# Performance work log

Measured on AMD Instinct MI355X. Metric: run time of the kernel, lower is better.

## Reference

```python
import jax, jax.numpy as jnp
import numpy as np

# dims matching init_kwargs / input_specs
B, C, H = 8, 256, 48          # input (B, C, H, H)
GRID = 3                       # sqrt(num_memory)
NUM_MEM = GRID * GRID          # 9
WS = H // GRID                 # window_size = 16
S = 128                        # num_slots
D = WS * WS * C                # slot_dim = 65536
K = 5                          # gumbel top-k threshold (shrink_thres, int)
EPS = 1e-12


def setup_inputs() -> dict:
    key = jax.random.key(0)
    k1, k2, k3 = jax.random.split(key, 3)
    stdv = 1.0 / np.sqrt(D)
    x = jax.random.normal(k1, (B, C, H, H), dtype=jnp.float32)
    mem1 = jax.random.uniform(k2, (NUM_MEM, S, D), jnp.float32, -stdv, stdv)
    mem2 = jax.random.uniform(k3, (NUM_MEM, S, D), jnp.float32, -stdv, stdv)
    return {"x": x, "mem1": mem1, "mem2": mem2}


def _window_partition(x):
    # (B, C, H, W) -> (B, NUM_MEM, WS*WS*C); per-window layout is (ws, ws, C) row-major,
    # matching torch unfold -> view(B,C,ws^2,L) -> permute(0,3,2,1).
    b = x.shape[0]
    x = jnp.transpose(x, (0, 2, 3, 1))                        # (B, H, W, C)
    x = x.reshape(b, GRID, WS, GRID, WS, C)
    x = jnp.transpose(x, (0, 1, 3, 2, 4, 5))                  # (B, gh, gw, ws, ws, C)
    return x.reshape(b, NUM_MEM, WS * WS * C)


def _window_reverse(w):
    # (B, NUM_MEM, WS*WS*C) -> (B, C, H, W); exact inverse of _window_partition.
    b = w.shape[0]
    w = w.reshape(b, GRID, GRID, WS, WS, C)
    w = jnp.transpose(w, (0, 1, 3, 2, 4, 5)).reshape(b, H, H, C)
    return jnp.transpose(w, (0, 3, 1, 2))


def _hard_shrink_relu(y, lambd):
    d = y - lambd
    return jax.nn.relu(d) * y / (jnp.abs(d) + EPS)


def _memory_read(q, mem):
    # q: (B, M, D) window queries; mem: (M, S, D) per-window memory matrices.
    att = jnp.einsum('bmd,msd->bms', q, mem)                  # (B, M, S)
    y = jax.nn.softmax(att, axis=-1)
    k = min(S - 1, K)
    thres = jax.lax.top_k(y, k)[0][..., -1:]                  # kth largest per row
    y_hard = _hard_shrink_relu(y, thres)
    y_hard = y_hard / jnp.maximum(jnp.sum(jnp.abs(y_hard), axis=-1, keepdims=True), EPS)
    y_hard = jax.lax.stop_gradient(y_hard - y) + y            # straight-through
    return jnp.einsum('bms,msd->bmd', y_hard, mem)            # (B, M, D)


def reference(x, mem1, mem2):
    # CRU modeled as identity split: x1 = x2 = x (CRU source not provided).
    q = _window_partition(x)                                  # (B, 9, D)
    out1 = _window_reverse(_memory_read(q, mem1))
    out2 = _window_reverse(_memory_read(q, mem2))
    return out1 + out2                                        # eval mode: no bernoulli mask
```

## Files before the change

kernel.cpp:

```cpp
#include <hip/hip_runtime.h>
#include <hip/hip_bf16.h>
#include <cstdint>

#define Bn 8
#define Cn 256
#define Hn 48
#define NUM_MEM 9
#define WSZ 16
#define Sn 128
#define Dn 65536
#define KTOP 5
#define NDC 128

__global__ __launch_bounds__(256) void k_x2q(const float* __restrict__ x,
                                             float* __restrict__ q) {
    const int h = blockIdx.x;
    const int b = blockIdx.y;
    const int gh = h >> 4, i = h & 15;
    __shared__ float tile[Cn * Hn];
    const float* xp = x + (size_t)b * Cn * Hn * Hn + (size_t)h * Hn;
    for (int o = threadIdx.x; o < Cn * Hn; o += blockDim.x) {
        int c = o / Hn, w = o - c * Hn;
        tile[o] = xp[(size_t)c * Hn * Hn + w];
    }
    __syncthreads();
    for (int gw = 0; gw < 3; ++gw) {
        float* qp = q + (size_t)(b * NUM_MEM + gh * 3 + gw) * Dn + i * (WSZ * Cn);
        for (int l = threadIdx.x; l < WSZ * Cn; l += blockDim.x) {
            int j = l >> 8, c = l & 255;
            qp[l] = tile[c * Hn + gw * WSZ + j];
        }
    }
}

__global__ __launch_bounds__(256) void k_att4(const float* __restrict__ q,
                                              const float* __restrict__ mem1,
                                              const float* __restrict__ mem2,
                                              float* __restrict__ ap) {
    const int dc = blockIdx.x;
    const int mw = blockIdx.y;
    const int sg = blockIdx.z;
    const int e  = sg >> 3;
    const int lane = threadIdx.x & 63, wave = threadIdx.x >> 6;
    const int s0 = (sg & 7) * 16 + wave * 4;

    const float4* mem4 = (const float4*)(e ? mem2 : mem1);
    const float4* q4   = (const float4*)q;
    const int off = dc * 128 + lane;

    float4 M[4][2];
#pragma unroll
    for (int r = 0; r < 4; ++r) {
        const float4* mp = mem4 + (size_t)(mw * Sn + s0 + r) * (Dn / 4) + off;
        M[r][0] = mp[0];
        M[r][1] = mp[64];
    }

    float a[32];
#pragma unroll
    for (int i = 0; i < 32; ++i) a[i] = 0.f;

#pragma unroll
    for (int half = 0; half < 2; ++half) {
        float4 Q[4][2];
#pragma unroll
        for (int b = 0; b < 4; ++b) {
            const float4* qp = q4 + (size_t)((half * 4 + b) * NUM_MEM + mw) * (Dn / 4) + off;
            Q[b][0] = qp[0];
            Q[b][1] = qp[64];
        }
#pragma unroll
        for (int r = 0; r < 4; ++r)
#pragma unroll
            for (int b = 0; b < 4; ++b) {
                const int bi = half * 4 + b;
                a[r * 8 + bi] += M[r][0].x * Q[b][0].x + M[r][0].y * Q[b][0].y
                               + M[r][0].z * Q[b][0].z + M[r][0].w * Q[b][0].w
                               + M[r][1].x * Q[b][1].x + M[r][1].y * Q[b][1].y
                               + M[r][1].z * Q[b][1].z + M[r][1].w * Q[b][1].w;
            }
    }

#pragma unroll
    for (int k = 0; k < 5; ++k) {
        const int mk = 1 << k;
        const bool up = (lane & mk) != 0;
#pragma unroll
        for (int j = 0; j < (32 >> (k + 1)); ++j) {
            float lo = a[2 * j], hi = a[2 * j + 1];
            float mine = up ? hi : lo;
            float oth  = __shfl_xor(up ? lo : hi, mk, 64);
            a[j] = mine + oth;
        }
    }
    float rsum = a[0] + __shfl_xor(a[0], 32, 64);
    if (lane < 32) {
        const int b = lane & 7, r = (lane >> 3) & 3;
        ap[((size_t)dc * 144 + (size_t)(e * 8 + b) * 9 + mw) * Sn + (s0 + r)] = rsum;
    }
}

__global__ __launch_bounds__(128) void k_smax(const float* __restrict__ ap,
                                              float* __restrict__ w) {
    const int row = blockIdx.x;
    const int t = threadIdx.x;
    __shared__ float sf[Sn];
    __shared__ unsigned long long sk[Sn];

    float v = 0.f;
#pragma unroll 8
    for (int nd = 0; nd < NDC; ++nd)
        v += ap[((size_t)nd * 144 + row) * Sn + t];

    sf[t] = v; __syncthreads();
    for (int s = 64; s > 0; s >>= 1) { if (t < s) sf[t] = fmaxf(sf[t], sf[t + s]); __syncthreads(); }
    float mx = sf[0]; __syncthreads();

    float e = expf(v - mx);
    sf[t] = e; __syncthreads();
    for (int s = 64; s > 0; s >>= 1) { if (t < s) sf[t] += sf[t + s]; __syncthreads(); }
    float sum = sf[0]; __syncthreads();
    float y = e / sum;

    bool alive = true;
    float thres = 0.f;
    unsigned int ybits = __float_as_uint(y);
    for (int it = 0; it < KTOP; ++it) {
        sk[t] = alive ? ((((unsigned long long)ybits) << 32) | (unsigned)t) : 0ull;
        __syncthreads();
        for (int s = 64; s > 0; s >>= 1) {
            if (t < s) { if (sk[t + s] > sk[t]) sk[t] = sk[t + s]; }
            __syncthreads();
        }
        unsigned long long kmax = sk[0];
        __syncthreads();
        if ((unsigned)(kmax & 0xffffffffull) == (unsigned)t) alive = false;
        thres = __uint_as_float((unsigned)(kmax >> 32));
    }

    float d   = y - thres;
    float num = fmaxf(d, 0.f) * y;
    float yh  = num / (fabsf(d) + 1e-12f);

    sf[t] = yh; __syncthreads();
    for (int s = 64; s > 0; s >>= 1) { if (t < s) sf[t] += sf[t + s]; __syncthreads(); }
    float l1 = sf[0];
    w[(size_t)row * Sn + t] = yh / fmaxf(l1, 1e-12f);
}

__global__ __launch_bounds__(256) void k_acc(const float* __restrict__ w,
                                             const float* __restrict__ mem1,
                                             const float* __restrict__ mem2,
                                             float* __restrict__ acc) {
    const int chunk = blockIdx.x;
    const int m     = blockIdx.y;
    const int b     = blockIdx.z;
    __shared__ int   nz[2];
    __shared__ int   idx[2][16];
    __shared__ float wv[2][16];
    if (threadIdx.x < 2) nz[threadIdx.x] = 0;
    __syncthreads();
    {
        int eidx = threadIdx.x >> 7;
        int s    = threadIdx.x & 127;
        float ww = w[((size_t)(eidx * Bn + b) * NUM_MEM + m) * Sn + s];
        if (ww != 0.f) {
            int p = atomicAdd(&nz[eidx], 1);
            if (p < 16) { idx[eidx][p] = s; wv[eidx][p] = ww; }
        }
    }
    __syncthreads();
    const int n1 = nz[0], n2 = nz[1];
    const size_t mbase = (size_t)m * Sn * Dn;
    const int dbase = chunk * 4096;
    for (int l = threadIdx.x * 4; l < 4096; l += 1024) {
        int d = dbase + l;
        float4 a = {0.f, 0.f, 0.f, 0.f};
        for (int j = 0; j < n1; ++j) {
            const float4 r = *(const float4*)(mem1 + mbase + (size_t)idx[0][j] * Dn + d);
            float ww = wv[0][j];
            a.x += ww * r.x; a.y += ww * r.y; a.z += ww * r.z; a.w += ww * r.w;
        }
        for (int j = 0; j < n2; ++j) {
            const float4 r = *(const float4*)(mem2 + mbase + (size_t)idx[1][j] * Dn + d);
            float ww = wv[1][j];
            a.x += ww * r.x; a.y += ww * r.y; a.z += ww * r.z; a.w += ww * r.w;
        }
        *(float4*)(acc + (size_t)(b * NUM_MEM + m) * Dn + d) = a;
    }
}

__global__ __launch_bounds__(256) void k_q2x(const float* __restrict__ acc,
                                             float* __restrict__ out) {
    const int h = blockIdx.x;
    const int b = blockIdx.y;
    const int gh = h >> 4, i = h & 15;
    __shared__ float tile[Cn * Hn];
    for (int gw = 0; gw < 3; ++gw) {
        const float* ap = acc + (size_t)(b * NUM_MEM + gh * 3 + gw) * Dn + i * (WSZ * Cn);
        for (int l = threadIdx.x; l < WSZ * Cn; l += blockDim.x) {
            int j = l >> 8, c = l & 255;
            tile[c * Hn + gw * WSZ + j] = ap[l];
        }
    }
    __syncthreads();
    float* op = out + (size_t)b * Cn * Hn * Hn + (size_t)h * Hn;
    for (int o = threadIdx.x; o < Cn * Hn; o += blockDim.x) {
        int c = o / Hn, wcol = o - c * Hn;
        op[(size_t)c * Hn * Hn + wcol] = tile[o];
    }
}

extern "C" void kernel_launch(void* const* d_in, const int* in_sizes, int n_in,
                              void* d_out, int out_size, void* d_ws, size_t ws_size,
                              hipStream_t stream) {
    const float* x    = (const float*)d_in[0];
    const float* mem1 = (const float*)d_in[1];
    const float* mem2 = (const float*)d_in[2];
    float* out = (float*)d_out;

    float* q    = (float*)d_ws;
    float* wbuf = q + (size_t)Bn * NUM_MEM * Dn;
    float* ap   = (float*)d_out;

    k_x2q<<<dim3(Hn, Bn), 256, 0, stream>>>(x, q);
    k_att4<<<dim3(NDC, NUM_MEM, 16), 256, 0, stream>>>(q, mem1, mem2, ap);
    k_smax<<<2 * Bn * NUM_MEM, 128, 0, stream>>>(ap, wbuf);
    k_acc<<<dim3(16, NUM_MEM, Bn), 256, 0, stream>>>(wbuf, mem1, mem2, q );
    k_q2x<<<dim3(Hn, Bn), 256, 0, stream>>>(q, out);
}
```

Measured before the change: 224.5 us.

## Restructure attention-score kernel with LDS double-buffered async memory loads and query reuse

The attention kernel now keeps all 8 batch queries in registers per block and loops over 8 slot groups. Memory rows are staged into LDS through global_load_lds with double buffering and explicit vmcnt waits. Query reads are no longer repeated across 8 slot-group blocks, and the memory stream is overlapped with compute. In exchange the grid is 8x smaller (2304 blocks) and each block carries many more registers, which may lower occupancy.

```diff
diff --git a/kernel.cpp b/kernel.cpp
--- a/kernel.cpp
+++ b/kernel.cpp
@@ -11,6 +11,10 @@
 #define Dn 65536
 #define KTOP 5
 #define NDC 128
+#define TW 512
+
+typedef const __attribute__((address_space(1))) uint32_t* gptr_t;
+typedef __attribute__((address_space(3))) uint32_t* lptr_t;
 
 __global__ __launch_bounds__(256) void k_x2q(const float* __restrict__ x,
                                              float* __restrict__ q) {
@@ -33,70 +37,82 @@
     }
 }
 
-__global__ __launch_bounds__(256) void k_att4(const float* __restrict__ q,
+__global__ __launch_bounds__(256) void k_att5(const float* __restrict__ q,
                                               const float* __restrict__ mem1,
                                               const float* __restrict__ mem2,
                                               float* __restrict__ ap) {
     const int dc = blockIdx.x;
     const int mw = blockIdx.y;
-    const int sg = blockIdx.z;
-    const int e  = sg >> 3;
+    const int e  = blockIdx.z;
     const int lane = threadIdx.x & 63, wave = threadIdx.x >> 6;
-    const int s0 = (sg & 7) * 16 + wave * 4;
-
-    const float4* mem4 = (const float4*)(e ? mem2 : mem1);
-    const float4* q4   = (const float4*)q;
-    const int off = dc * 128 + lane;
-
-    float4 M[4][2];
-#pragma unroll
-    for (int r = 0; r < 4; ++r) {
-        const float4* mp = mem4 + (size_t)(mw * Sn + s0 + r) * (Dn / 4) + off;
-        M[r][0] = mp[0];
-        M[r][1] = mp[64];
-    }
-
-    float a[32];
-#pragma unroll
-    for (int i = 0; i < 32; ++i) a[i] = 0.f;
-
-#pragma unroll
-    for (int half = 0; half < 2; ++half) {
-        float4 Q[4][2];
-#pragma unroll
-        for (int b = 0; b < 4; ++b) {
-            const float4* qp = q4 + (size_t)((half * 4 + b) * NUM_MEM + mw) * (Dn / 4) + off;
-            Q[b][0] = qp[0];
-            Q[b][1] = qp[64];
-        }
-#pragma unroll
-        for (int r = 0; r < 4; ++r)
-#pragma unroll
-            for (int b = 0; b < 4; ++b) {
-                const int bi = half * 4 + b;
-                a[r * 8 + bi] += M[r][0].x * Q[b][0].x + M[r][0].y * Q[b][0].y
-                               + M[r][0].z * Q[b][0].z + M[r][0].w * Q[b][0].w
-                               + M[r][1].x * Q[b][1].x + M[r][1].y * Q[b][1].y
-                               + M[r][1].z * Q[b][1].z + M[r][1].w * Q[b][1].w;
+
+    const float* mem = e ? mem2 : mem1;
+    const float4* q4 = (const float4*)q;
+
+    __shared__ float lds[4][2][4][TW];
+
+    float4 Q[8][2];
+#pragma unroll
+    for (int b = 0; b < 8; ++b) {
+        const size_t qb = (size_t)(b * NUM_MEM + mw) * (Dn / 4) + (size_t)dc * (TW / 4);
+        Q[b][0] = q4[qb + lane];
+        Q[b][1] = q4[qb + 64 + lane];
+    }
+
+    auto stage = [&](int t, int buf) {
+#pragma unroll
+        for (int u = 0; u < 8; ++u) {
+            const int r = u >> 1, half = u & 1;
+            const float* src = mem + ((size_t)(mw * Sn + t * 16 + wave * 4 + r)) * Dn
+                             + (size_t)dc * TW + half * 256 + lane * 4;
+            __builtin_amdgcn_global_load_lds((gptr_t)src,
+                                             (lptr_t)&lds[wave][buf][r][half * 256],
+                                             16, 0, 0);
+        }
+    };
+
+    stage(0, 0);
+
+    for (int t = 0; t < 8; ++t) {
+        const int buf = t & 1;
+        if (t < 7) stage(t + 1, buf ^ 1);
+
+        if (t < 7) { asm volatile("s_waitcnt vmcnt(8)" ::: "memory"); }
+        else       { asm volatile("s_waitcnt vmcnt(0)" ::: "memory"); }
+        __builtin_amdgcn_sched_barrier(0);
+
+        float a[32];
+#pragma unroll
+        for (int r = 0; r < 4; ++r) {
+            float4 m0 = *(const float4*)&lds[wave][buf][r][lane * 4];
+            float4 m1 = *(const float4*)&lds[wave][buf][r][256 + lane * 4];
+#pragma unroll
+            for (int b = 0; b < 8; ++b) {
+                a[r * 8 + b] = m0.x * Q[b][0].x + m0.y * Q[b][0].y
+                             + m0.z * Q[b][0].z + m0.w * Q[b][0].w
+                             + m1.x * Q[b][1].x + m1.y * Q[b][1].y
+                             + m1.z * Q[b][1].z + m1.w * Q[b][1].w;
             }
-    }
-
-#pragma unroll
-    for (int k = 0; k < 5; ++k) {
-        const int mk = 1 << k;
-        const bool up = (lane & mk) != 0;
-#pragma unroll
-        for (int j = 0; j < (32 >> (k + 1)); ++j) {
-            float lo = a[2 * j], hi = a[2 * j + 1];
-            float mine = up ? hi : lo;
-            float oth  = __shfl_xor(up ? lo : hi, mk, 64);
-            a[j] = mine + oth;
-        }
-    }
-    float rsum = a[0] + __shfl_xor(a[0], 32, 64);
-    if (lane < 32) {
-        const int b = lane & 7, r = (lane >> 3) & 3;
-        ap[((size_t)dc * 144 + (size_t)(e * 8 + b) * 9 + mw) * Sn + (s0 + r)] = rsum;
+        }
+
+#pragma unroll
+        for (int k = 0; k < 5; ++k) {
+            const int mk = 1 << k;
+            const bool up = (lane & mk) != 0;
+#pragma unroll
+            for (int j = 0; j < (32 >> (k + 1)); ++j) {
+                float lo = a[2 * j], hi = a[2 * j + 1];
+                float mine = up ? hi : lo;
+                float oth  = __shfl_xor(up ? lo : hi, mk, 64);
+                a[j] = mine + oth;
+            }
+        }
+        float rsum = a[0] + __shfl_xor(a[0], 32, 64);
+        if (lane < 32) {
+            const int b = lane & 7, r = (lane >> 3) & 3;
+            const int s = t * 16 + wave * 4 + r;
+            ap[((size_t)dc * 144 + (size_t)(e * 8 + b) * 9 + mw) * Sn + s] = rsum;
+        }
     }
 }
 
@@ -224,7 +240,7 @@
     float* ap   = (float*)d_out;
 
     k_x2q<<<dim3(Hn, Bn), 256, 0, stream>>>(x, q);
-    k_att4<<<dim3(NDC, NUM_MEM, 16), 256, 0, stream>>>(q, mem1, mem2, ap);
+    k_att5<<<dim3(NDC, NUM_MEM, 2), 256, 0, stream>>>(q, mem1, mem2, ap);
     k_smax<<<2 * Bn * NUM_MEM, 128, 0, stream>>>(ap, wbuf);
     k_acc<<<dim3(16, NUM_MEM, Bn), 256, 0, stream>>>(wbuf, mem1, mem2, q );
     k_q2x<<<dim3(Hn, Bn), 256, 0, stream>>>(q, out);
```

Measured after the change: 220.3 us. About the same (-1.9%).
